# Kernel optimization log

Measured on AMD Instinct MI355X. Metric: run time of the kernel, lower is better.

## Reference

```python
import jax, jax.numpy as jnp
import numpy as np

FIELDS, NUM, CAT = 39, 13, 26
D, M, V, B, DEEP = 16, 16, 100000, 4096, 400
LEFT, RIGHT = np.triu_indices(FIELDS, k=1)  # pair indices, Q = 741
Q = LEFT.size
EPS = 1e-5


def setup_inputs() -> dict:
    key = jax.random.key(0)
    ks = jax.random.split(key, 18)
    xi = jax.random.randint(ks[0], (B, CAT), 0, V)
    xv = jax.random.uniform(ks[1], (B, NUM), dtype=jnp.float32)
    # 2nd-order embedding tables, stacked since all fields share vocab size
    emb_tables = jax.random.normal(ks[2], (FIELDS, V, D), dtype=jnp.float32) * 0.1
    T3 = jax.random.normal(ks[3], (D, M, D), dtype=jnp.float32) * 0.05
    T2 = jax.random.normal(ks[4], (M, D * D), dtype=jnp.float32) * 0.05
    gc = jax.random.normal(ks[5], (Q,), dtype=jnp.float32)
    fi_w = jax.random.normal(ks[6], (Q * M, DEEP), dtype=jnp.float32) * 0.01
    fi_b = jnp.zeros((DEEP,), dtype=jnp.float32)
    fi_gamma = jnp.ones((DEEP,), dtype=jnp.float32)
    fi_beta = jnp.zeros((DEEP,), dtype=jnp.float32)
    emb_w = jax.random.normal(ks[7], (FIELDS * D, DEEP), dtype=jnp.float32) * 0.02
    emb_b = jnp.zeros((DEEP,), dtype=jnp.float32)
    emb_gamma = jnp.ones((DEEP,), dtype=jnp.float32)
    emb_beta = jnp.zeros((DEEP,), dtype=jnp.float32)
    fc_w = jax.random.normal(ks[8], (2 * DEEP, 1), dtype=jnp.float32) * 0.05
    fc_b = jnp.zeros((1,), dtype=jnp.float32)
    return {"xi": xi, "xv": xv, "emb_tables": emb_tables, "T3": T3, "T2": T2,
            "gc": gc, "fi_w": fi_w, "fi_b": fi_b, "fi_gamma": fi_gamma, "fi_beta": fi_beta,
            "emb_w": emb_w, "emb_b": emb_b, "emb_gamma": emb_gamma, "emb_beta": emb_beta,
            "fc_w": fc_w, "fc_b": fc_b}


def _bn(x, gamma, beta):
    # BatchNorm1d in training mode: batch statistics, biased variance
    mean = jnp.mean(x, axis=0)
    var = jnp.var(x, axis=0)
    return gamma * (x - mean) * jax.lax.rsqrt(var + EPS) + beta


def reference(xi, xv, emb_tables, T3, T2, gc, fi_w, fi_b, fi_gamma, fi_beta,
              emb_w, emb_b, emb_gamma, emb_beta, fc_w, fc_b):
    # numerical fields: embedding row 0 scaled by the raw value
    num_part = xv[:, :, None] * emb_tables[:NUM, 0, :][None]          # [B, 13, D]
    # categorical fields: per-field gather
    cat_part = emb_tables[NUM + jnp.arange(CAT)[None, :], xi]          # [B, 26, D]
    fm2 = jnp.concatenate([num_part, cat_part], axis=1)               # [B, 39, D]
    vi = fm2[:, LEFT]                                                  # [B, Q, D]
    vj = fm2[:, RIGHT]                                                 # [B, Q, D]
    # einsum('bqd,dmd,bqd->bm'): repeated d on T3 takes its diagonal -> [D, M]
    T3diag = jnp.einsum('dmd->dm', T3)
    ga = jnp.einsum('bqd,bqd,dm->bm', vi, vj, T3diag)                  # [B, M]
    ga = jax.nn.softmax(ga, axis=1)
    # T1 = einsum('bm,mn->bmn'); s = einsum('bqd,bmn,bqd->bqm') sums T1 over n
    t1_rowsum = ga * jnp.sum(T2, axis=1)[None, :]                      # [B, M]
    pair_dot = jnp.einsum('bqd,bqd->bq', vi, vj)                       # [B, Q]
    s = pair_dot[:, :, None] * t1_rowsum[:, None, :]                   # [B, Q, M]
    sh = (s * gc[None, :, None]).reshape(-1, Q * M)                    # [B, Q*M]
    th = jax.nn.relu(_bn(sh @ fi_w + fi_b, fi_gamma, fi_beta))         # [B, DEEP]
    emb = fm2.reshape(-1, FIELDS * D)                                  # [B, 39*D]
    emb = jax.nn.relu(_bn(emb @ emb_w + emb_b, emb_gamma, emb_beta))   # [B, DEEP]
    out = jnp.concatenate([th, emb], axis=1) @ fc_w + fc_b             # [B, 1]
    return jnp.sum(jax.nn.sigmoid(out), axis=1)                        # [B]
```

## Files before the change

kernel.cpp:

```cpp
#include <hip/hip_runtime.h>
#include <hip/hip_bf16.h>

#define BATCH 4096
#define FIELDS_ 39
#define NUMF 13
#define CATF 26
#define DD 16
#define MM 16
#define VV 100000
#define DEEP_ 400
#define QQ 741
#define QPAD 768
#define KE 624
#define KEP 640
#define NEP 512
#define N1 6400
#define NKTE 20
#define NT_ 24
#define EPS_ 1e-5f

#define OFF_ABF 0
#define OFF_T   (BATCH*QPAD/2)
#define OFF_W2  (OFF_T + BATCH*MM)
#define OFF_WE  (OFF_W2 + N1*QPAD/2)
#define OFF_FMB (OFF_WE + NEP*KEP/2)
#define OFF_TH  (OFF_FMB + BATCH*KEP/2)
#define OFF_EMB (OFF_TH + BATCH*DEEP_)
#define OFF_ACC (OFF_EMB + BATCH*DEEP_)
#define OFF_T2S (OFF_ACC + 1600)
#define OFF_T3D (OFF_T2S + 16)

typedef __attribute__((ext_vector_type(8))) short bf16x8;
typedef __attribute__((ext_vector_type(4))) float f32x4;

__device__ __forceinline__ ushort f2bf(float v) {
    union { float f; unsigned u; } x; x.f = v;
    unsigned r = x.u + 0x7fff + ((x.u >> 16) & 1);
    return (ushort)(r >> 16);
}
__device__ __forceinline__ unsigned pack2(float a, float b) {
    return (unsigned)f2bf(a) | ((unsigned)f2bf(b) << 16);
}
__device__ __forceinline__ void async16(void* lds, const void* g) {
    __builtin_amdgcn_global_load_lds(
        (const __attribute__((address_space(1))) unsigned int*)g,
        (__attribute__((address_space(3))) unsigned int*)lds,
        16, 0, 0);
}

__global__ __launch_bounds__(256) void kprep0(const float* __restrict__ T3,
                                              const float* __restrict__ T2,
                                              float* __restrict__ ws) {
    int tid = threadIdx.x;
    if (tid < MM) {
        float s = 0.f;
        for (int j = 0; j < DD * DD; ++j) s += T2[tid * DD * DD + j];
        ws[OFF_T2S + tid] = s;
    }
    if (tid < DD * MM) {
        int d = tid >> 4, m = tid & 15;
        ws[OFF_T3D + tid] = T3[(d * MM + m) * DD + d];
    }
    for (int i = tid; i < 1600; i += 256) ws[OFF_ACC + i] = 0.f;
}

__global__ __launch_bounds__(256) void kbig(const int* __restrict__ xi,
                                            const float* __restrict__ xv,
                                            const float* __restrict__ emb,
                                            const float* __restrict__ gc,
                                            const float* __restrict__ fi_w,
                                            const float* __restrict__ emb_w,
                                            float* __restrict__ ws,
                                            ushort* __restrict__ Abf,
                                            ushort* __restrict__ FMB,
                                            ushort* __restrict__ W2,
                                            ushort* __restrict__ WE) {
    __shared__ float smem[4200];
    int bid = blockIdx.x, tid = threadIdx.x;

    if (bid < BATCH) {
        float* row = smem;
        float* hsh = smem + 624;
        float* gash = smem + 640;
        ushort* stA = (ushort*)(smem + 656);
        ushort* stF = stA + QPAD;
        int b = bid;
        for (int e = tid; e < KE; e += 256) {
            int f = e >> 4, d = e & 15;
            float v;
            if (f < NUMF) {
                v = xv[b * NUMF + f] * emb[(long)f * VV * DD + d];
            } else {
                int c = f - NUMF;
                int idxv = xi[b * CATF + c];
                v = emb[((long)(NUMF + c) * VV + idxv) * DD + d];
            }
            row[e] = v;
        }
        __syncthreads();
        for (int e = tid; e < KEP; e += 256)
            stF[e] = (e < KE) ? f2bf(row[e]) : (ushort)0;
        if (tid < DD) {
            float s = 0.f, s2 = 0.f;
            for (int f = 0; f < FIELDS_; ++f) { float v = row[f * DD + tid]; s += v; s2 += v * v; }
            hsh[tid] = 0.5f * (s * s - s2);
        }
        __syncthreads();
        if (tid < MM) {
            float g = 0.f;
            for (int d = 0; d < DD; ++d) g += hsh[d] * ws[OFF_T3D + d * MM + tid];
            gash[tid] = g;
        }
        __syncthreads();
        if (tid < MM) {
            float mx = -1e30f;
            for (int m = 0; m < MM; ++m) mx = fmaxf(mx, gash[m]);
            float se = 0.f;
            for (int m = 0; m < MM; ++m) se += expf(gash[m] - mx);
            ws[OFF_T + b * MM + tid] = expf(gash[tid] - mx) / se * ws[OFF_T2S + tid];
        }
        for (int q = tid; q < QPAD; q += 256) {
            float av = 0.f;
            if (q < QQ) {
                int i = 0, qq = q, cnt = FIELDS_ - 1;
                while (qq >= cnt) { qq -= cnt; ++i; cnt = FIELDS_ - 1 - i; }
                int j = i + 1 + qq;
                float dot = 0.f;
#pragma unroll
                for (int d = 0; d < DD; ++d) dot += row[i * DD + d] * row[j * DD + d];
                av = dot * gc[q];
            }
            stA[q] = f2bf(av);
        }
        __syncthreads();
        if (tid < 96)
            *(uint4*)&Abf[(long)b * QPAD + tid * 8] = *(uint4*)&stA[tid * 8];
        else if (tid < 176)
            *(uint4*)&FMB[(long)b * KEP + (tid - 96) * 8] = *(uint4*)&stF[(tid - 96) * 8];
    } else if (bid < BATCH + 1536) {
        int bt = bid - BATCH;
        int kt = bt >> 6, m = (bt >> 2) & 15, ch = bt & 3;
        float* tile = smem;
        for (int i = tid; i < 32 * 25; i += 256) {
            int ql = i / 25, c4 = i - ql * 25;
            int q = kt * 32 + ql;
            float4 v = make_float4(0.f, 0.f, 0.f, 0.f);
            if (q < QQ) v = *(const float4*)&fi_w[(q * MM + m) * DEEP_ + ch * 100 + c4 * 4];
            tile[ql * 101 + c4 * 4 + 0] = v.x; tile[ql * 101 + c4 * 4 + 1] = v.y;
            tile[ql * 101 + c4 * 4 + 2] = v.z; tile[ql * 101 + c4 * 4 + 3] = v.w;
        }
        __syncthreads();
        for (int i = tid; i < 100 * 4; i += 256) {
            int lc = i >> 2, cq = i & 3;
            int kcol = ch * 100 + lc;
            unsigned r[4];
#pragma unroll
            for (int j = 0; j < 4; ++j)
                r[j] = pack2(tile[(cq * 8 + 2 * j) * 101 + lc], tile[(cq * 8 + 2 * j + 1) * 101 + lc]);
            *(uint4*)&W2[(long)(kcol * 16 + m) * QPAD + kt * 32 + cq * 8] =
                make_uint4(r[0], r[1], r[2], r[3]);
        }
    } else {
        int bt = bid - BATCH - 1536;
        int kt = bt >> 2, ch = bt & 3;
        float* tile = smem;
        for (int i = tid; i < 32 * 32; i += 256) {
            int kl = i >> 5, c4 = i & 31;
            int k = kt * 32 + kl;
            int n = ch * 128 + c4 * 4;
            float4 v = make_float4(0.f, 0.f, 0.f, 0.f);
            if (k < KE && n < DEEP_) v = *(const float4*)&emb_w[k * DEEP_ + n];
            tile[kl * 129 + c4 * 4 + 0] = v.x; tile[kl * 129 + c4 * 4 + 1] = v.y;
            tile[kl * 129 + c4 * 4 + 2] = v.z; tile[kl * 129 + c4 * 4 + 3] = v.w;
        }
        __syncthreads();
        for (int i = tid; i < 128 * 4; i += 256) {
            int nl = i >> 2, cq = i & 3;
            int n = ch * 128 + nl;
            uint4 o = make_uint4(0, 0, 0, 0);
            if (n < DEEP_) {
                unsigned r[4];
#pragma unroll
                for (int j = 0; j < 4; ++j)
                    r[j] = pack2(tile[(cq * 8 + 2 * j) * 129 + nl], tile[(cq * 8 + 2 * j + 1) * 129 + nl]);
                o = make_uint4(r[0], r[1], r[2], r[3]);
            }
            if (n < NEP)
                *(uint4*)&WE[(long)n * KEP + kt * 32 + cq * 8] = o;
        }
    }
}

__device__ __forceinline__ void pipeline3(const ushort* p0, const ushort* p1,
                                          const ushort* p2, const ushort* p3,
                                          ushort* lds, int tid, int nt,
                                          int f1b, int f2b, int sw,
                                          f32x4 (*acc)[4]) {
#define STAGEP(SL, T) { \
    ushort* L_ = lds + (SL) * 16384; \
    async16(L_ + tid * 8,         p0 + (T) * 32); \
    async16(L_ + 4096 + tid * 8,  p1 + (T) * 32); \
    async16(L_ + 8192 + tid * 8,  p2 + (T) * 32); \
    async16(L_ + 12288 + tid * 8, p3 + (T) * 32); }
    STAGEP(0, 0); STAGEP(1, 1);
    asm volatile("s_waitcnt vmcnt(4)" ::: "memory");
    __builtin_amdgcn_s_barrier();
    int sl = 0;
    for (int t = 0; t < nt; ++t) {
        __builtin_amdgcn_sched_barrier(0);
        const ushort* cur = lds + sl * 16384;
        bf16x8 f1[8], f2[4];
#pragma unroll
        for (int r = 0; r < 8; ++r) f1[r] = *(const bf16x8*)&cur[f1b + r * 512 + sw];
#pragma unroll
        for (int c = 0; c < 4; ++c) f2[c] = *(const bf16x8*)&cur[f2b + c * 512 + sw];
        int sl2 = sl + 2; if (sl2 >= 3) sl2 -= 3;
        if (t + 2 < nt) STAGEP(sl2, t + 2);
        __builtin_amdgcn_s_setprio(1);
#pragma unroll
        for (int r = 0; r < 8; ++r)
#pragma unroll
            for (int c = 0; c < 4; ++c)
                acc[r][c] = __builtin_amdgcn_mfma_f32_16x16x32_bf16(f1[r], f2[c], acc[r][c], 0, 0, 0);
        __builtin_amdgcn_s_setprio(0);
        if (t + 1 < nt) {
            if (t + 2 < nt) { asm volatile("s_waitcnt vmcnt(4)" ::: "memory"); }
            else            { asm volatile("s_waitcnt vmcnt(0)" ::: "memory"); }
            __builtin_amdgcn_s_barrier();
        }
        sl = sl + 1; if (sl >= 3) sl -= 3;
    }
#undef STAGEP
}

__global__ __launch_bounds__(512, 2) void kgemms(const ushort* __restrict__ Abf,
                                                 const ushort* __restrict__ W2,
                                                 const ushort* __restrict__ FMB,
                                                 const ushort* __restrict__ WE,
                                                 const float* __restrict__ Tmat,
                                                 float* __restrict__ TH,
                                                 float* __restrict__ EMB,
                                                 float* __restrict__ ACC) {
    __shared__ ushort ldsbuf[3 * 16384];
    __shared__ float red[512];
    int tid = threadIdx.x;
    int lane = tid & 63, wid = tid >> 6;
    int wB = wid >> 2;
    int wS = wid & 3;
    int kq = lane >> 4, lr = lane & 15;
    int rr = tid >> 2, ac = tid & 3;
    int csw = (ac ^ ((rr >> 1) & 3)) * 8;
    int sw = (kq ^ ((lr >> 1) & 3)) * 8;
    red[tid] = 0.f;
    f32x4 acc[8][4] = {};
    int wg = blockIdx.x;

    if (wg < 400) {
        int s = (wg & 7) * 50 + (wg >> 3);
        int b0 = (s / 25) * 256;
        int n0 = (s % 25) * 256;
        const ushort* p0 = Abf + (long)(b0 + rr) * QPAD + csw;
        const ushort* p1 = Abf + (long)(b0 + 128 + rr) * QPAD + csw;
        const ushort* p2 = W2 + (long)(n0 + rr) * QPAD + csw;
        const ushort* p3 = W2 + (long)(n0 + 128 + rr) * QPAD + csw;
        pipeline3(p0, p1, p2, p3, ldsbuf, tid, NT_,
                  8192 + (wB * 128 + lr) * 32, (wS * 64 + lr) * 32, sw, acc);
        float* tbuf = (float*)ldsbuf;
        float ls[8] = {}, ls2[8] = {};
#pragma unroll
        for (int cg = 0; cg < 4; ++cg) {
            int bloc = wS * 64 + cg * 16 + lr;
            float4 t4 = *(const float4*)&Tmat[(b0 + bloc) * 16 + kq * 4];
#pragma unroll
            for (int r = 0; r < 8; ++r) {
                float v = acc[r][cg][0] * t4.x + acc[r][cg][1] * t4.y +
                          acc[r][cg][2] * t4.z + acc[r][cg][3] * t4.w;
                v += __shfl_xor(v, 16);
                v += __shfl_xor(v, 32);
                ls[r] += v; ls2[r] += v * v;
                if (lane < 16) tbuf[bloc * 17 + wB * 8 + r] = v;
            }
        }
#pragma unroll
        for (int r = 0; r < 8; ++r) {
            float a = ls[r], b2 = ls2[r];
            a += __shfl_xor(a, 8, 16); b2 += __shfl_xor(b2, 8, 16);
            a += __shfl_xor(a, 4, 16); b2 += __shfl_xor(b2, 4, 16);
            a += __shfl_xor(a, 2, 16); b2 += __shfl_xor(b2, 2, 16);
            a += __shfl_xor(a, 1, 16); b2 += __shfl_xor(b2, 1, 16);
            if (lane == 0) {
                atomicAdd(&red[wB * 8 + r], a);
                atomicAdd(&red[16 + wB * 8 + r], b2);
            }
        }
        __syncthreads();
        if (tid < 16) {
            atomicAdd(&ACC[(n0 >> 4) + tid], red[tid]);
            atomicAdd(&ACC[800 + (n0 >> 4) + tid], red[16 + tid]);
        }
        {
            int rowl = tid >> 1, kcb = (tid & 1) * 8;
            float o0 = tbuf[rowl * 17 + kcb + 0];
            float o1 = tbuf[rowl * 17 + kcb + 1];
            float o2 = tbuf[rowl * 17 + kcb + 2];
            float o3 = tbuf[rowl * 17 + kcb + 3];
            float o4 = tbuf[rowl * 17 + kcb + 4];
            float o5 = tbuf[rowl * 17 + kcb + 5];
            float o6 = tbuf[rowl * 17 + kcb + 6];
            float o7 = tbuf[rowl * 17 + kcb + 7];
            float* dst = &TH[(b0 + rowl) * DEEP_ + (n0 >> 4) + kcb];
            *(float4*)dst = make_float4(o0, o1, o2, o3);
            *(float4*)(dst + 4) = make_float4(o4, o5, o6, o7);
        }
    } else {
        int e = wg - 400;
        int se = (e & 7) * 4 + (e >> 3);
        int b0 = (se >> 1) * 256;
        int n0 = (se & 1) * 256;
        const ushort* p0 = FMB + (long)(b0 + rr) * KEP + csw;
        const ushort* p1 = FMB + (long)(b0 + 128 + rr) * KEP + csw;
        const ushort* p2 = WE + (long)(n0 + rr) * KEP + csw;
        const ushort* p3 = WE + (long)(n0 + 128 + rr) * KEP + csw;
        pipeline3(p0, p1, p2, p3, ldsbuf, tid, NKTE,
                  (wB * 128 + lr) * 32, 8192 + (wS * 64 + lr) * 32, sw, acc);
#pragma unroll
        for (int cg = 0; cg < 4; ++cg) {
            int ncl = wS * 64 + cg * 16 + lr;
            int nc = n0 + ncl;
            float ls = 0.f, ls2 = 0.f;
#pragma unroll
            for (int r = 0; r < 8; ++r) {
#pragma unroll
                for (int j = 0; j < 4; ++j) {
                    float v = acc[r][cg][j];
                    int brow = b0 + wB * 128 + r * 16 + kq * 4 + j;
                    if (nc < DEEP_) EMB[brow * DEEP_ + nc] = v;
                    ls += v; ls2 += v * v;
                }
            }
            ls += __shfl_xor(ls, 16);  ls += __shfl_xor(ls, 32);
            ls2 += __shfl_xor(ls2, 16); ls2 += __shfl_xor(ls2, 32);
            if (lane < 16 && nc < DEEP_) {
                atomicAdd(&red[ncl], ls);
                atomicAdd(&red[256 + ncl], ls2);
            }
        }
        __syncthreads();
        if (tid < 256) {
            int nc = n0 + tid;
            if (nc < DEEP_) {
                atomicAdd(&ACC[400 + nc], red[tid]);
                atomicAdd(&ACC[1200 + nc], red[256 + tid]);
            }
        }
    }
}

__global__ __launch_bounds__(256) void kfinal(const float* __restrict__ fig,
                                              const float* __restrict__ fibeta,
                                              const float* __restrict__ eg,
                                              const float* __restrict__ ebeta,
                                              const float* __restrict__ fcw,
                                              const float* __restrict__ fcb,
                                              const float* __restrict__ ws,
                                              float* __restrict__ out) {
    int b = blockIdx.x, tid = threadIdx.x;
    float part = 0.f;
    if (tid < 200) {
        int c = tid * 4;
        int loc = (c < DEEP_) ? c : c - DEEP_;
        const float* xp = (c < DEEP_) ? &ws[OFF_TH + b * DEEP_ + loc]
                                      : &ws[OFF_EMB + b * DEEP_ + loc];
        float4 x = *(const float4*)xp;
        float4 g = *(const float4*)((c < DEEP_) ? &fig[loc] : &eg[loc]);
        float4 be = *(const float4*)((c < DEEP_) ? &fibeta[loc] : &ebeta[loc]);
        float4 sm = *(const float4*)&ws[OFF_ACC + c];
        float4 sq = *(const float4*)&ws[OFF_ACC + 800 + c];
        float4 w = *(const float4*)&fcw[c];
        const float* xv_ = (const float*)&x; const float* gv = (const float*)&g;
        const float* bev = (const float*)&be; const float* smv = (const float*)&sm;
        const float* sqv = (const float*)&sq; const float* wv = (const float*)&w;
#pragma unroll
        for (int j = 0; j < 4; ++j) {
            float mean = smv[j] * (1.f / BATCH);
            float var = sqv[j] * (1.f / BATCH) - mean * mean;
            float rstd = rsqrtf(var + EPS_);
            float v = fmaxf(gv[j] * (xv_[j] - mean) * rstd + bev[j], 0.f);
            part += v * wv[j];
        }
    }
    __shared__ float red[4];
#pragma unroll
    for (int off = 32; off > 0; off >>= 1) part += __shfl_down(part, off, 64);
    if ((tid & 63) == 0) red[tid >> 6] = part;
    __syncthreads();
    if (tid == 0) {
        float tot = red[0] + red[1] + red[2] + red[3] + fcb[0];
        out[b] = 1.f / (1.f + expf(-tot));
    }
}

extern "C" void kernel_launch(void* const* d_in, const int* in_sizes, int n_in,
                              void* d_out, int out_size, void* d_ws, size_t ws_size,
                              hipStream_t stream) {
    const int*   xi    = (const int*)d_in[0];
    const float* xv    = (const float*)d_in[1];
    const float* emb   = (const float*)d_in[2];
    const float* T3    = (const float*)d_in[3];
    const float* T2    = (const float*)d_in[4];
    const float* gc    = (const float*)d_in[5];
    const float* fi_w  = (const float*)d_in[6];
    const float* fig   = (const float*)d_in[8];
    const float* fibt  = (const float*)d_in[9];
    const float* emb_w = (const float*)d_in[10];
    const float* eg    = (const float*)d_in[12];
    const float* ebt   = (const float*)d_in[13];
    const float* fcw   = (const float*)d_in[14];
    const float* fcb   = (const float*)d_in[15];
    float* ws = (float*)d_ws;
    ushort* Abf = (ushort*)(ws + OFF_ABF);
    ushort* W2  = (ushort*)(ws + OFF_W2);
    ushort* WE  = (ushort*)(ws + OFF_WE);
    ushort* FMB = (ushort*)(ws + OFF_FMB);
    float* out = (float*)d_out;

    hipLaunchKernelGGL(kprep0, dim3(1), dim3(256), 0, stream, T3, T2, ws);
    hipLaunchKernelGGL(kbig, dim3(BATCH + 1536 + 80), dim3(256), 0, stream,
                       xi, xv, emb, gc, fi_w, emb_w, ws, Abf, FMB, W2, WE);
    hipLaunchKernelGGL(kgemms, dim3(432), dim3(512), 0, stream,
                       Abf, W2, FMB, WE, ws + OFF_T, ws + OFF_TH, ws + OFF_EMB, ws + OFF_ACC);
    hipLaunchKernelGGL(kfinal, dim3(BATCH), dim3(256), 0, stream,
                       fig, fibt, eg, ebt, fcw, fcb, ws, out);
}
```

Measured before the change: 89.47 us.

## Deepen GEMM pipeline to four LDS stages with double-buffered register fragments

```diff
diff --git a/kernel.cpp b/kernel.cpp
--- a/kernel.cpp
+++ b/kernel.cpp
@@ -191,49 +191,58 @@
     }
 }
 
-__device__ __forceinline__ void pipeline3(const ushort* p0, const ushort* p1,
+#define SLOTU 16384
+__device__ __forceinline__ void pipeline4(const ushort* p0, const ushort* p1,
                                           const ushort* p2, const ushort* p3,
                                           ushort* lds, int tid, int nt,
                                           int f1b, int f2b, int sw,
                                           f32x4 (*acc)[4]) {
 #define STAGEP(SL, T) { \
-    ushort* L_ = lds + (SL) * 16384; \
+    ushort* L_ = lds + (SL) * SLOTU; \
     async16(L_ + tid * 8,         p0 + (T) * 32); \
     async16(L_ + 4096 + tid * 8,  p1 + (T) * 32); \
     async16(L_ + 8192 + tid * 8,  p2 + (T) * 32); \
     async16(L_ + 12288 + tid * 8, p3 + (T) * 32); }
-    STAGEP(0, 0); STAGEP(1, 1);
+#define READ1(F, SL) { const ushort* C_ = lds + (SL) * SLOTU; \
+    _Pragma("unroll") for (int r_ = 0; r_ < 8; ++r_) F[r_] = *(const bf16x8*)&C_[f1b + r_ * 512 + sw]; }
+#define READ2(F, SL) { const ushort* C_ = lds + (SL) * SLOTU; \
+    _Pragma("unroll") for (int c_ = 0; c_ < 4; ++c_) F[c_] = *(const bf16x8*)&C_[f2b + c_ * 512 + sw]; }
+#define MF(FA, FB) { __builtin_amdgcn_s_setprio(1); \
+    _Pragma("unroll") for (int r_ = 0; r_ < 8; ++r_) \
+    _Pragma("unroll") for (int c_ = 0; c_ < 4; ++c_) \
+        acc[r_][c_] = __builtin_amdgcn_mfma_f32_16x16x32_bf16(FA[r_], FB[c_], acc[r_][c_], 0, 0, 0); \
+    __builtin_amdgcn_s_setprio(0); }
+
+    bf16x8 f1A[8], f2A[4], f1B[8], f2B[4];
+    STAGEP(0, 0); STAGEP(1, 1); STAGEP(2, 2);
     asm volatile("s_waitcnt vmcnt(4)" ::: "memory");
     __builtin_amdgcn_s_barrier();
-    int sl = 0;
-    for (int t = 0; t < nt; ++t) {
+    READ1(f1A, 0); READ2(f2A, 0);
+    for (int t = 0; t < nt; t += 2) {
         __builtin_amdgcn_sched_barrier(0);
-        const ushort* cur = lds + sl * 16384;
-        bf16x8 f1[8], f2[4];
-#pragma unroll
-        for (int r = 0; r < 8; ++r) f1[r] = *(const bf16x8*)&cur[f1b + r * 512 + sw];
-#pragma unroll
-        for (int c = 0; c < 4; ++c) f2[c] = *(const bf16x8*)&cur[f2b + c * 512 + sw];
-        int sl2 = sl + 2; if (sl2 >= 3) sl2 -= 3;
-        if (t + 2 < nt) STAGEP(sl2, t + 2);
-        __builtin_amdgcn_s_setprio(1);
-#pragma unroll
-        for (int r = 0; r < 8; ++r)
-#pragma unroll
-            for (int c = 0; c < 4; ++c)
-                acc[r][c] = __builtin_amdgcn_mfma_f32_16x16x32_bf16(f1[r], f2[c], acc[r][c], 0, 0, 0);
-        __builtin_amdgcn_s_setprio(0);
-        if (t + 1 < nt) {
-            if (t + 2 < nt) { asm volatile("s_waitcnt vmcnt(4)" ::: "memory"); }
+        READ1(f1B, (t + 1) & 3); READ2(f2B, (t + 1) & 3);
+        if (t + 3 < nt) STAGEP((t + 3) & 3, t + 3);
+        MF(f1A, f2A);
+        if (t + 3 < nt) { asm volatile("s_waitcnt vmcnt(4)" ::: "memory"); }
+        else            { asm volatile("s_waitcnt vmcnt(0)" ::: "memory"); }
+        __builtin_amdgcn_s_barrier();
+        __builtin_amdgcn_sched_barrier(0);
+        if (t + 2 < nt) { READ1(f1A, (t + 2) & 3); READ2(f2A, (t + 2) & 3); }
+        if (t + 4 < nt) STAGEP((t + 4) & 3, t + 4);
+        MF(f1B, f2B);
+        if (t + 2 < nt) {
+            if (t + 4 < nt) { asm volatile("s_waitcnt vmcnt(4)" ::: "memory"); }
             else            { asm volatile("s_waitcnt vmcnt(0)" ::: "memory"); }
             __builtin_amdgcn_s_barrier();
         }
-        sl = sl + 1; if (sl >= 3) sl -= 3;
     }
 #undef STAGEP
-}
-
-__global__ __launch_bounds__(512, 2) void kgemms(const ushort* __restrict__ Abf,
+#undef READ1
+#undef READ2
+#undef MF
+}
+
+__global__ __launch_bounds__(512, 1) void kgemms(const ushort* __restrict__ Abf,
                                                  const ushort* __restrict__ W2,
                                                  const ushort* __restrict__ FMB,
                                                  const ushort* __restrict__ WE,
@@ -241,7 +250,7 @@
                                                  float* __restrict__ TH,
                                                  float* __restrict__ EMB,
                                                  float* __restrict__ ACC) {
-    __shared__ ushort ldsbuf[3 * 16384];
+    __shared__ ushort ldsbuf[4 * SLOTU];
     __shared__ float red[512];
     int tid = threadIdx.x;
     int lane = tid & 63, wid = tid >> 6;
@@ -263,7 +272,7 @@
         const ushort* p1 = Abf + (long)(b0 + 128 + rr) * QPAD + csw;
         const ushort* p2 = W2 + (long)(n0 + rr) * QPAD + csw;
         const ushort* p3 = W2 + (long)(n0 + 128 + rr) * QPAD + csw;
-        pipeline3(p0, p1, p2, p3, ldsbuf, tid, NT_,
+        pipeline4(p0, p1, p2, p3, ldsbuf, tid, NT_,
                   8192 + (wB * 128 + lr) * 32, (wS * 64 + lr) * 32, sw, acc);
         float* tbuf = (float*)ldsbuf;
         float ls[8] = {}, ls2[8] = {};
@@ -321,7 +330,7 @@
         const ushort* p1 = FMB + (long)(b0 + 128 + rr) * KEP + csw;
         const ushort* p2 = WE + (long)(n0 + rr) * KEP + csw;
         const ushort* p3 = WE + (long)(n0 + 128 + rr) * KEP + csw;
-        pipeline3(p0, p1, p2, p3, ldsbuf, tid, NKTE,
+        pipeline4(p0, p1, p2, p3, ldsbuf, tid, NKTE,
                   (wB * 128 + lr) * 32, 8192 + (wS * 64 + lr) * 32, sw, acc);
 #pragma unroll
         for (int cg = 0; cg < 4; ++cg) {
```

Result: slower. 92.03 us (+2.9%).

## Fold prep kernel into kbig and move T2 row-sum scaling into W2 weights

Applied to the files above, without the earlier changes.

```diff
diff --git a/kernel.cpp b/kernel.cpp
--- a/kernel.cpp
+++ b/kernel.cpp
@@ -27,8 +27,6 @@
 #define OFF_TH  (OFF_FMB + BATCH*KEP/2)
 #define OFF_EMB (OFF_TH + BATCH*DEEP_)
 #define OFF_ACC (OFF_EMB + BATCH*DEEP_)
-#define OFF_T2S (OFF_ACC + 1600)
-#define OFF_T3D (OFF_T2S + 16)
 
 typedef __attribute__((ext_vector_type(8))) short bf16x8;
 typedef __attribute__((ext_vector_type(4))) float f32x4;
@@ -46,22 +44,6 @@
         (const __attribute__((address_space(1))) unsigned int*)g,
         (__attribute__((address_space(3))) unsigned int*)lds,
         16, 0, 0);
-}
-
-__global__ __launch_bounds__(256) void kprep0(const float* __restrict__ T3,
-                                              const float* __restrict__ T2,
-                                              float* __restrict__ ws) {
-    int tid = threadIdx.x;
-    if (tid < MM) {
-        float s = 0.f;
-        for (int j = 0; j < DD * DD; ++j) s += T2[tid * DD * DD + j];
-        ws[OFF_T2S + tid] = s;
-    }
-    if (tid < DD * MM) {
-        int d = tid >> 4, m = tid & 15;
-        ws[OFF_T3D + tid] = T3[(d * MM + m) * DD + d];
-    }
-    for (int i = tid; i < 1600; i += 256) ws[OFF_ACC + i] = 0.f;
 }
 
 __global__ __launch_bounds__(256) void kbig(const int* __restrict__ xi,
@@ -70,6 +52,8 @@
                                             const float* __restrict__ gc,
                                             const float* __restrict__ fi_w,
                                             const float* __restrict__ emb_w,
+                                            const float* __restrict__ T3,
+                                            const float* __restrict__ T2,
                                             float* __restrict__ ws,
                                             ushort* __restrict__ Abf,
                                             ushort* __restrict__ FMB,
@@ -108,7 +92,7 @@
         __syncthreads();
         if (tid < MM) {
             float g = 0.f;
-            for (int d = 0; d < DD; ++d) g += hsh[d] * ws[OFF_T3D + d * MM + tid];
+            for (int d = 0; d < DD; ++d) g += hsh[d] * T3[(d * MM + tid) * DD + d];
             gash[tid] = g;
         }
         __syncthreads();
@@ -117,7 +101,7 @@
             for (int m = 0; m < MM; ++m) mx = fmaxf(mx, gash[m]);
             float se = 0.f;
             for (int m = 0; m < MM; ++m) se += expf(gash[m] - mx);
-            ws[OFF_T + b * MM + tid] = expf(gash[tid] - mx) / se * ws[OFF_T2S + tid];
+            ws[OFF_T + b * MM + tid] = expf(gash[tid] - mx) / se;
         }
         for (int q = tid; q < QPAD; q += 256) {
             float av = 0.f;
@@ -125,9 +109,14 @@
                 int i = 0, qq = q, cnt = FIELDS_ - 1;
                 while (qq >= cnt) { qq -= cnt; ++i; cnt = FIELDS_ - 1 - i; }
                 int j = i + 1 + qq;
-                float dot = 0.f;
-#pragma unroll
-                for (int d = 0; d < DD; ++d) dot += row[i * DD + d] * row[j * DD + d];
+                const float4* ri = (const float4*)&row[i * DD];
+                const float4* rj = (const float4*)&row[j * DD];
+                float4 a0 = ri[0], a1 = ri[1], a2 = ri[2], a3 = ri[3];
+                float4 b0 = rj[0], b1 = rj[1], b2 = rj[2], b3 = rj[3];
+                float dot = a0.x * b0.x + a0.y * b0.y + a0.z * b0.z + a0.w * b0.w
+                          + a1.x * b1.x + a1.y * b1.y + a1.z * b1.z + a1.w * b1.w
+                          + a2.x * b2.x + a2.y * b2.y + a2.z * b2.z + a2.w * b2.w
+                          + a3.x * b3.x + a3.y * b3.y + a3.z * b3.z + a3.w * b3.w;
                 av = dot * gc[q];
             }
             stA[q] = f2bf(av);
@@ -141,6 +130,12 @@
         int bt = bid - BATCH;
         int kt = bt >> 6, m = (bt >> 2) & 15, ch = bt & 3;
         float* tile = smem;
+        {
+            float p = T2[m * DD * DD + tid];
+#pragma unroll
+            for (int off = 32; off > 0; off >>= 1) p += __shfl_down(p, off, 64);
+            if ((tid & 63) == 0) smem[4100 + (tid >> 6)] = p;
+        }
         for (int i = tid; i < 32 * 25; i += 256) {
             int ql = i / 25, c4 = i - ql * 25;
             int q = kt * 32 + ql;
@@ -150,18 +145,23 @@
             tile[ql * 101 + c4 * 4 + 2] = v.z; tile[ql * 101 + c4 * 4 + 3] = v.w;
         }
         __syncthreads();
+        float t2s = smem[4100] + smem[4101] + smem[4102] + smem[4103];
         for (int i = tid; i < 100 * 4; i += 256) {
             int lc = i >> 2, cq = i & 3;
             int kcol = ch * 100 + lc;
             unsigned r[4];
 #pragma unroll
             for (int j = 0; j < 4; ++j)
-                r[j] = pack2(tile[(cq * 8 + 2 * j) * 101 + lc], tile[(cq * 8 + 2 * j + 1) * 101 + lc]);
+                r[j] = pack2(tile[(cq * 8 + 2 * j) * 101 + lc] * t2s,
+                             tile[(cq * 8 + 2 * j + 1) * 101 + lc] * t2s);
             *(uint4*)&W2[(long)(kcol * 16 + m) * QPAD + kt * 32 + cq * 8] =
                 make_uint4(r[0], r[1], r[2], r[3]);
         }
     } else {
         int bt = bid - BATCH - 1536;
+        if (bt == 0) {
+            for (int i = tid; i < 1600; i += 256) ws[OFF_ACC + i] = 0.f;
+        }
         int kt = bt >> 2, ch = bt & 3;
         float* tile = smem;
         for (int i = tid; i < 32 * 32; i += 256) {
@@ -424,9 +424,8 @@
     ushort* FMB = (ushort*)(ws + OFF_FMB);
     float* out = (float*)d_out;
 
-    hipLaunchKernelGGL(kprep0, dim3(1), dim3(256), 0, stream, T3, T2, ws);
     hipLaunchKernelGGL(kbig, dim3(BATCH + 1536 + 80), dim3(256), 0, stream,
-                       xi, xv, emb, gc, fi_w, emb_w, ws, Abf, FMB, W2, WE);
+                       xi, xv, emb, gc, fi_w, emb_w, T3, T2, ws, Abf, FMB, W2, WE);
     hipLaunchKernelGGL(kgemms, dim3(432), dim3(512), 0, stream,
                        Abf, W2, FMB, WE, ws + OFF_T, ws + OFF_TH, ws + OFF_EMB, ws + OFF_ACC);
     hipLaunchKernelGGL(kfinal, dim3(BATCH), dim3(256), 0, stream,
```

Result: faster. 83.74 us (-6.4%).
